# Performance work log

Hardware: AMD Instinct MI355X
Metric: run time of the kernel (lower is better)

The kernel has to match this reference:

```python
import jax, jax.numpy as jnp
import numpy as np

N_NODES = 50000


def _gcn_conv(h, src, dst, W, b):
    # h: [N, d_in] -> [N, d_out]; symmetric-normalized aggregation with self-loops
    N = h.shape[0]
    h = h @ W  # transform first (d_out < d_in), like PyG GCNConv
    deg = jax.ops.segment_sum(jnp.ones_like(dst, dtype=h.dtype), dst, num_segments=N)
    dinv = jnp.where(deg > 0, jax.lax.rsqrt(jnp.maximum(deg, 1.0)), 0.0)
    norm = dinv[src] * dinv[dst]  # [E']
    msg = h[src] * norm[:, None]  # [E', d_out]
    out = jax.ops.segment_sum(msg, dst, num_segments=N)
    return out + b


def setup_inputs() -> dict:
    key = jax.random.key(0)
    k1, k2, k3, k4 = jax.random.split(key, 4)
    dim_in, dim_h, dim_out, E = 512, 96, 40, 800000
    x = jax.random.normal(k1, (N_NODES, dim_in), dtype=jnp.float32)
    edge_index = jax.random.randint(k2, (2, E), 0, N_NODES, dtype=jnp.int64)
    W1 = jax.random.normal(k3, (dim_in, dim_h), dtype=jnp.float32) / np.sqrt(dim_in)
    b1 = jnp.zeros((dim_h,), dtype=jnp.float32)
    W2 = jax.random.normal(k4, (dim_h, dim_out), dtype=jnp.float32) / np.sqrt(dim_h)
    b2 = jnp.zeros((dim_out,), dtype=jnp.float32)
    return {"x": x, "edge_index": edge_index, "W1": W1, "b1": b1, "W2": W2, "b2": b2}


def reference(x, edge_index, W1, b1, W2, b2):
    N = x.shape[0]
    loops = jnp.arange(N, dtype=edge_index.dtype)
    src = jnp.concatenate([edge_index[0], loops])
    dst = jnp.concatenate([edge_index[1], loops])
    h = jax.nn.relu(_gcn_conv(x, src, dst, W1, b1))
    # dropout p=0.5 is identity in eval mode (training=False)
    logits = _gcn_conv(h, src, dst, W2, b2)
    return (logits, jax.nn.log_softmax(logits, axis=1))
```

## Files before the change

kernel.cpp:

```cpp
#include <hip/hip_runtime.h>
#include <hip/hip_bf16.h>
#include <cstdint>
#include <cstddef>

#define DIN 512
#define DH  96
#define DOUT 40

typedef __attribute__((ext_vector_type(8))) short s8v;
typedef __attribute__((ext_vector_type(4))) float f4v;

__device__ __forceinline__ ushort f2bf(float f) {
    uint u = __float_as_uint(f);
    u += 0x7fffu + ((u >> 16) & 1u);
    return (ushort)(u >> 16);
}
__device__ __forceinline__ uint f2bf2(float lo, float hi) {
    __hip_bfloat162 h = __float22bfloat162_rn(make_float2(lo, hi));
    return *(uint*)&h;
}
__device__ __forceinline__ float bflo(uint u) { return __uint_as_float(u << 16); }
__device__ __forceinline__ float bfhi(uint u) { return __uint_as_float(u & 0xffff0000u); }

__global__ __launch_bounds__(256) void k_prep(
    const float* __restrict__ W1, const float* __restrict__ W2,
    int* __restrict__ cnt, ushort* __restrict__ W1T, ushort* __restrict__ W2T, int N)
{
    int i = blockIdx.x * 256 + threadIdx.x;
    if (i < N) cnt[i] = 0;
    if (i < DIN * DH) {
        int k = i / DH, n = i % DH;
        W1T[(size_t)n * DIN + k] = f2bf(W1[i]);
    }
    if (i < 48 * DH) {
        int n = i / DH, k = i % DH;
        W2T[i] = (n < DOUT) ? f2bf(W2[(size_t)k * DOUT + n]) : (ushort)0;
    }
}

__global__ __launch_bounds__(256) void k_hist(
    const int* __restrict__ dst, int* __restrict__ cnt, int* __restrict__ pos, int E)
{
    int e = blockIdx.x * 256 + threadIdx.x;
    if (e < E) pos[e] = atomicAdd(&cnt[dst[e]], 1);
}

__global__ __launch_bounds__(256) void k_rowptr_all(
    const int* __restrict__ cnt, int* __restrict__ row_ptr,
    float* __restrict__ dinv, int N)
{
    __shared__ int p[256];
    __shared__ int wred[4];
    const int tid = threadIdx.x, b = blockIdx.x;

    int pre = 0;
    const int limit = b * 256;
    for (int j = tid; j < limit; j += 256) pre += cnt[j];
    #pragma unroll
    for (int off = 32; off >= 1; off >>= 1) pre += __shfl_down(pre, off, 64);
    if ((tid & 63) == 0) wred[tid >> 6] = pre;
    __syncthreads();
    const int base0 = wred[0] + wred[1] + wred[2] + wred[3];

    int i = b * 256 + tid;
    int c = (i < N) ? cnt[i] : 0;
    p[tid] = c;
    __syncthreads();
    #pragma unroll
    for (int off = 1; off < 256; off <<= 1) {
        int t = (tid >= off) ? p[tid - off] : 0;
        __syncthreads();
        p[tid] += t;
        __syncthreads();
    }
    int excl = p[tid] - c;
    if (i < N) {
        int base = base0 + excl;
        row_ptr[i] = base;
        dinv[i] = rsqrtf(1.0f + (float)c);
        if (i == N - 1) row_ptr[N] = base + c;
    }
}

__global__ __launch_bounds__(256) void k_fill(
    const int* __restrict__ src, const int* __restrict__ dst,
    const int* __restrict__ row_ptr, const int* __restrict__ pos,
    int* __restrict__ adj, int E)
{
    int e = blockIdx.x * 256 + threadIdx.x;
    if (e >= E) return;
    adj[row_ptr[dst[e]] + pos[e]] = src[e];
}

#define SWZ(r) (((r >> 1) & 3) << 3)
__global__ __launch_bounds__(256) void k_gemm1(
    const float* __restrict__ x, const ushort* __restrict__ W1T,
    const float* __restrict__ dinv, ushort* __restrict__ hs1, int N)
{
    __shared__ __align__(16) ushort lds[10240];
    const int tid = threadIdx.x;
    const int row0 = blockIdx.x * 64;
    const int lane = tid & 63, w = tid >> 6;
    const int rb = (w >> 1) * 32, cb = (w & 1) * 48;
    const int lm = lane & 15, lq = lane >> 4;

    int aof[2], bof[3];
    #pragma unroll
    for (int i = 0; i < 2; ++i) {
        int r = rb + i * 16 + lm;
        aof[i] = r * 32 + ((lq * 8) ^ SWZ(r));
    }
    #pragma unroll
    for (int j = 0; j < 3; ++j) {
        int n = cb + j * 16 + lm;
        bof[j] = 4096 + n * 32 + ((lq * 8) ^ SWZ(n));
    }

    f4v acc[2][3];
    #pragma unroll
    for (int i = 0; i < 2; ++i)
        #pragma unroll
        for (int j = 0; j < 3; ++j) acc[i][j] = (f4v)0.f;

    const int sr = tid >> 2;
    const int c0 = (tid & 3) * 8;

    auto stage = [&](int kt, int buf) {
        int k0 = kt * 32;
        int gr = row0 + sr;
        ushort* A = lds + buf * 2048;
        float4 v0 = make_float4(0.f, 0.f, 0.f, 0.f), v1 = v0;
        if (gr < N) {
            const float* pp = &x[(size_t)gr * DIN + k0 + c0];
            v0 = *(const float4*)pp;
            v1 = *(const float4*)(pp + 4);
        }
        uint4 wv;
        wv.x = f2bf2(v0.x, v0.y);
        wv.y = f2bf2(v0.z, v0.w);
        wv.z = f2bf2(v1.x, v1.y);
        wv.w = f2bf2(v1.z, v1.w);
        *(uint4*)&A[sr * 32 + (c0 ^ SWZ(sr))] = wv;
        ushort* B = lds + 4096 + buf * 3072;
        #pragma unroll
        for (int f = tid; f < 384; f += 256) {
            int n = f >> 2, cc = (f & 3) * 8;
            uint4 bv = *(const uint4*)&W1T[(size_t)n * DIN + k0 + cc];
            *(uint4*)&B[n * 32 + (cc ^ SWZ(n))] = bv;
        }
    };

    stage(0, 0);
    for (int kt = 0; kt < 16; ++kt) {
        __syncthreads();
        if (kt < 15) stage(kt + 1, (kt + 1) & 1);
        const int ab = (kt & 1) * 2048;
        const int bb = (kt & 1) * 3072;
        s8v b0 = *(s8v*)&lds[bof[0] + bb];
        s8v b1 = *(s8v*)&lds[bof[1] + bb];
        s8v b2 = *(s8v*)&lds[bof[2] + bb];
        #pragma unroll
        for (int i = 0; i < 2; ++i) {
            s8v a = *(s8v*)&lds[aof[i] + ab];
            acc[i][0] = __builtin_amdgcn_mfma_f32_16x16x32_bf16(a, b0, acc[i][0], 0, 0, 0);
            acc[i][1] = __builtin_amdgcn_mfma_f32_16x16x32_bf16(a, b1, acc[i][1], 0, 0, 0);
            acc[i][2] = __builtin_amdgcn_mfma_f32_16x16x32_bf16(a, b2, acc[i][2], 0, 0, 0);
        }
    }

    #pragma unroll
    for (int i = 0; i < 2; ++i) {
        int gr0 = row0 + rb + i * 16 + lq * 4;
        #pragma unroll
        for (int q = 0; q < 4; ++q) {
            int gr = gr0 + q;
            if (gr < N) {
                float di = dinv[gr];
                #pragma unroll
                for (int j = 0; j < 3; ++j)
                    hs1[(size_t)gr * DH + cb + j * 16 + lm] = f2bf(acc[i][j][q] * di);
            }
        }
    }
}

__global__ __launch_bounds__(256) void k_agg1(
    const int* __restrict__ row_ptr, const int* __restrict__ adj,
    const float* __restrict__ dinv, const ushort* __restrict__ hs1,
    const float* __restrict__ b1, ushort* __restrict__ h1, int N)
{
    int t = blockIdx.x * 256 + threadIdx.x;
    int node = t >> 6, lane = t & 63;
    if (node >= N) return;
    int c = lane << 1;
    const bool act = (c < DH);

    float a0 = 0.f, a1 = 0.f;
    if (act) {
        uint u = *(const uint*)&hs1[(size_t)node * DH + c];
        a0 = bflo(u); a1 = bfhi(u);
    }
    int e = row_ptr[node], e1 = row_ptr[node + 1];
    for (; e + 7 < e1; e += 8) {
        int s0 = adj[e],     s1 = adj[e + 1], s2 = adj[e + 2], s3 = adj[e + 3];
        int s4 = adj[e + 4], s5 = adj[e + 5], s6 = adj[e + 6], s7 = adj[e + 7];
        if (act) {
            uint u0 = *(const uint*)&hs1[(size_t)s0 * DH + c];
            uint u1 = *(const uint*)&hs1[(size_t)s1 * DH + c];
            uint u2 = *(const uint*)&hs1[(size_t)s2 * DH + c];
            uint u3 = *(const uint*)&hs1[(size_t)s3 * DH + c];
            uint u4 = *(const uint*)&hs1[(size_t)s4 * DH + c];
            uint u5 = *(const uint*)&hs1[(size_t)s5 * DH + c];
            uint u6 = *(const uint*)&hs1[(size_t)s6 * DH + c];
            uint u7 = *(const uint*)&hs1[(size_t)s7 * DH + c];
            a0 += bflo(u0); a1 += bfhi(u0);
            a0 += bflo(u1); a1 += bfhi(u1);
            a0 += bflo(u2); a1 += bfhi(u2);
            a0 += bflo(u3); a1 += bfhi(u3);
            a0 += bflo(u4); a1 += bfhi(u4);
            a0 += bflo(u5); a1 += bfhi(u5);
            a0 += bflo(u6); a1 += bfhi(u6);
            a0 += bflo(u7); a1 += bfhi(u7);
        }
    }
    for (; e < e1; ++e) {
        int s = adj[e];
        if (act) {
            uint u = *(const uint*)&hs1[(size_t)s * DH + c];
            a0 += bflo(u); a1 += bfhi(u);
        }
    }
    if (act) {
        float di = dinv[node];
        float r0 = fmaxf(fmaf(a0, di, b1[c]), 0.f);
        float r1 = fmaxf(fmaf(a1, di, b1[c + 1]), 0.f);
        *(uint*)&h1[(size_t)node * DH + c] = f2bf2(r0, r1);
    }
}

__global__ __launch_bounds__(256) void k_gemm2(
    const ushort* __restrict__ h1, const ushort* __restrict__ W2T,
    const float* __restrict__ dinv, ushort* __restrict__ hs2b, int N)
{
    __shared__ __align__(16) ushort lds[16384 + 48 * 128];
    const int tid = threadIdx.x;
    const int row0 = blockIdx.x * 128;

    for (int f = tid; f < 576; f += 256) {
        int r = f / 12, c = (f % 12) * 8;
        uint4 v = *(const uint4*)&W2T[r * DH + c];
        *(uint4*)&lds[16384 + r * 128 + (c ^ ((r & 7) << 3))] = v;
    }
    {
        int r = tid >> 1, half = tid & 1;
        int gr = row0 + r;
        #pragma unroll
        for (int i = 0; i < 6; ++i) {
            int c = half * 48 + i * 8;
            uint4 v = make_uint4(0, 0, 0, 0);
            if (gr < N) v = *(const uint4*)&h1[(size_t)gr * DH + c];
            *(uint4*)&lds[r * 128 + (c ^ ((r & 7) << 3))] = v;
        }
    }
    __syncthreads();

    const int lane = tid & 63, w = tid >> 6;
    const int rb = w * 32, lm = lane & 15, lq = lane >> 4;
    f4v acc[2][3];
    #pragma unroll
    for (int i = 0; i < 2; ++i)
        #pragma unroll
        for (int j = 0; j < 3; ++j) acc[i][j] = (f4v)0.f;

    #pragma unroll
    for (int ks = 0; ks < 3; ++ks) {
        int kk = ks * 32 + lq * 8;
        s8v b[3];
        #pragma unroll
        for (int j = 0; j < 3; ++j) {
            int n = j * 16 + lm;
            b[j] = *(s8v*)&lds[16384 + n * 128 + (kk ^ ((n & 7) << 3))];
        }
        #pragma unroll
        for (int i = 0; i < 2; ++i) {
            int r = rb + i * 16 + lm;
            s8v a = *(s8v*)&lds[r * 128 + (kk ^ ((r & 7) << 3))];
            #pragma unroll
            for (int j = 0; j < 3; ++j)
                acc[i][j] = __builtin_amdgcn_mfma_f32_16x16x32_bf16(a, b[j], acc[i][j], 0, 0, 0);
        }
    }

    #pragma unroll
    for (int i = 0; i < 2; ++i) {
        int gr0 = row0 + rb + i * 16 + lq * 4;
        #pragma unroll
        for (int q = 0; q < 4; ++q) {
            int gr = gr0 + q;
            if (gr < N) {
                float di = dinv[gr];
                #pragma unroll
                for (int j = 0; j < 3; ++j) {
                    int col = j * 16 + lm;
                    if (col < DOUT)
                        hs2b[(size_t)gr * 64 + col] = f2bf(acc[i][j][q] * di);
                }
            }
        }
    }
}

__global__ __launch_bounds__(256) void k_agg2sm(
    const int* __restrict__ row_ptr, const int* __restrict__ adj,
    const float* __restrict__ dinv, const ushort* __restrict__ hs2b,
    const float* __restrict__ b2, float* __restrict__ out,
    float* __restrict__ lsm, int N)
{
    int t = blockIdx.x * 256 + threadIdx.x;
    int node = t >> 6, lane = t & 63;
    if (node >= N) return;
    int c = lane << 1;
    const bool act = (c < DOUT);

    float a0 = 0.f, a1 = 0.f;
    if (act) {
        uint u = *(const uint*)&hs2b[(size_t)node * 64 + c];
        a0 = bflo(u); a1 = bfhi(u);
    }
    int e = row_ptr[node], e1 = row_ptr[node + 1];
    for (; e + 7 < e1; e += 8) {
        int s0 = adj[e],     s1 = adj[e + 1], s2 = adj[e + 2], s3 = adj[e + 3];
        int s4 = adj[e + 4], s5 = adj[e + 5], s6 = adj[e + 6], s7 = adj[e + 7];
        if (act) {
            uint u0 = *(const uint*)&hs2b[(size_t)s0 * 64 + c];
            uint u1 = *(const uint*)&hs2b[(size_t)s1 * 64 + c];
            uint u2 = *(const uint*)&hs2b[(size_t)s2 * 64 + c];
            uint u3 = *(const uint*)&hs2b[(size_t)s3 * 64 + c];
            uint u4 = *(const uint*)&hs2b[(size_t)s4 * 64 + c];
            uint u5 = *(const uint*)&hs2b[(size_t)s5 * 64 + c];
            uint u6 = *(const uint*)&hs2b[(size_t)s6 * 64 + c];
            uint u7 = *(const uint*)&hs2b[(size_t)s7 * 64 + c];
            a0 += bflo(u0); a1 += bfhi(u0);
            a0 += bflo(u1); a1 += bfhi(u1);
            a0 += bflo(u2); a1 += bfhi(u2);
            a0 += bflo(u3); a1 += bfhi(u3);
            a0 += bflo(u4); a1 += bfhi(u4);
            a0 += bflo(u5); a1 += bfhi(u5);
            a0 += bflo(u6); a1 += bfhi(u6);
            a0 += bflo(u7); a1 += bfhi(u7);
        }
    }
    for (; e < e1; ++e) {
        int s = adj[e];
        if (act) {
            uint u = *(const uint*)&hs2b[(size_t)s * 64 + c];
            a0 += bflo(u); a1 += bfhi(u);
        }
    }

    float di = act ? dinv[node] : 0.f;
    float v0 = act ? fmaf(a0, di, b2[c]) : -1e30f;
    float v1 = act ? fmaf(a1, di, b2[c + 1]) : -1e30f;
    float m = fmaxf(v0, v1);
    #pragma unroll
    for (int off = 32; off >= 1; off >>= 1) m = fmaxf(m, __shfl_xor(m, off));
    float ex = act ? (__expf(v0 - m) + __expf(v1 - m)) : 0.f;
    float s = ex;
    #pragma unroll
    for (int off = 32; off >= 1; off >>= 1) s += __shfl_xor(s, off);
    float lse = m + __logf(s);
    if (act) {
        *(float2*)&out[(size_t)node * DOUT + c] = make_float2(v0, v1);
        *(float2*)&lsm[(size_t)node * DOUT + c] = make_float2(v0 - lse, v1 - lse);
    }
}

extern "C" void kernel_launch(void* const* d_in, const int* in_sizes, int n_in,
                              void* d_out, int out_size, void* d_ws, size_t ws_size,
                              hipStream_t stream) {
    const float* x  = (const float*)d_in[0];
    const int*   ei = (const int*)d_in[1];
    const float* W1 = (const float*)d_in[2];
    const float* b1 = (const float*)d_in[3];
    const float* W2 = (const float*)d_in[4];
    const float* b2 = (const float*)d_in[5];

    const int N = in_sizes[0] / DIN;
    const int E = in_sizes[1] / 2;
    const int* srcp = ei;
    const int* dstp = ei + E;
    const int SB = (N + 255) / 256;

    ushort* hs1  = (ushort*)d_ws;
    ushort* h1   = hs1 + (size_t)N * DH;
    ushort* hs2b = h1 + (size_t)N * DH;
    float* dinv  = (float*)(hs2b + (size_t)N * 64);
    ushort* W1T  = (ushort*)(dinv + N);
    ushort* W2T  = W1T + (size_t)DH * DIN;
    int* cnt     = (int*)(W2T + 48 * DH);
    int* row_ptr = cnt + N;
    int* adj     = row_ptr + N + 1;
    int* pos     = adj + E;

    float* out = (float*)d_out;
    float* lsm = out + (size_t)N * DOUT;

    const int gE = (E + 255) / 256;

    k_prep<<<SB, 256, 0, stream>>>(W1, W2, cnt, W1T, W2T, N);
    k_hist<<<gE, 256, 0, stream>>>(dstp, cnt, pos, E);
    k_rowptr_all<<<SB, 256, 0, stream>>>(cnt, row_ptr, dinv, N);
    k_fill<<<gE, 256, 0, stream>>>(srcp, dstp, row_ptr, pos, adj, E);

    k_gemm1<<<(N + 63) / 64, 256, 0, stream>>>(x, W1T, dinv, hs1, N);
    k_agg1<<<(int)(((size_t)N * 64 + 255) / 256), 256, 0, stream>>>(row_ptr, adj, dinv, hs1, b1, h1, N);

    k_gemm2<<<(N + 127) / 128, 256, 0, stream>>>(h1, W2T, dinv, hs2b, N);
    k_agg2sm<<<(int)(((size_t)N * 64 + 255) / 256), 256, 0, stream>>>(row_ptr, adj, dinv, hs2b, b2, out, lsm, N);
}
```

Before: 203.8 us.

## Enlarge GEMM1 row tile to 128 and prefetch global tiles into registers

The first GEMM now covers 128 rows per block instead of 64, so each wave computes four 16-row MFMA tiles and every W1 tile staged in LDS is reused across twice as many rows. Global loads for the next k-step are issued into registers right after the barrier, and the bf16 conversion and LDS store happen at the start of the next iteration, so load latency overlaps the MFMA work. The cost is more registers per thread and fewer blocks (about 391 for 50k rows), which may leave part of the GPU underused.

```diff
diff --git a/kernel.cpp b/kernel.cpp
--- a/kernel.cpp
+++ b/kernel.cpp
@@ -97,70 +97,87 @@
     const float* __restrict__ x, const ushort* __restrict__ W1T,
     const float* __restrict__ dinv, ushort* __restrict__ hs1, int N)
 {
-    __shared__ __align__(16) ushort lds[10240];
+    __shared__ __align__(16) ushort lds[14336];
     const int tid = threadIdx.x;
-    const int row0 = blockIdx.x * 64;
+    const int row0 = blockIdx.x * 128;
     const int lane = tid & 63, w = tid >> 6;
-    const int rb = (w >> 1) * 32, cb = (w & 1) * 48;
+    const int rb = (w >> 1) * 64, cb = (w & 1) * 48;
     const int lm = lane & 15, lq = lane >> 4;
 
-    int aof[2], bof[3];
-    #pragma unroll
-    for (int i = 0; i < 2; ++i) {
+    int aof[4], bof[3];
+    #pragma unroll
+    for (int i = 0; i < 4; ++i) {
         int r = rb + i * 16 + lm;
         aof[i] = r * 32 + ((lq * 8) ^ SWZ(r));
     }
     #pragma unroll
     for (int j = 0; j < 3; ++j) {
         int n = cb + j * 16 + lm;
-        bof[j] = 4096 + n * 32 + ((lq * 8) ^ SWZ(n));
-    }
-
-    f4v acc[2][3];
-    #pragma unroll
-    for (int i = 0; i < 2; ++i)
+        bof[j] = 8192 + n * 32 + ((lq * 8) ^ SWZ(n));
+    }
+
+    f4v acc[4][3];
+    #pragma unroll
+    for (int i = 0; i < 4; ++i)
         #pragma unroll
         for (int j = 0; j < 3; ++j) acc[i][j] = (f4v)0.f;
 
-    const int sr = tid >> 2;
-    const int c0 = (tid & 3) * 8;
-
-    auto stage = [&](int kt, int buf) {
+    const int sr = tid >> 1, c0 = (tid & 1) * 16;
+    const int bn0 = tid >> 2, bc0 = (tid & 3) * 8;
+    const int bn1 = (tid + 256) >> 2, bc1 = (tid & 3) * 8;
+    const bool hasB1 = tid < 128;
+    const int gr = row0 + sr;
+    const bool grok = gr < N;
+
+    float4 ra[2][2];
+    uint4 rb0, rb1;
+
+    auto load_regs = [&](int kt) {
         int k0 = kt * 32;
-        int gr = row0 + sr;
-        ushort* A = lds + buf * 2048;
-        float4 v0 = make_float4(0.f, 0.f, 0.f, 0.f), v1 = v0;
-        if (gr < N) {
-            const float* pp = &x[(size_t)gr * DIN + k0 + c0];
-            v0 = *(const float4*)pp;
-            v1 = *(const float4*)(pp + 4);
-        }
-        uint4 wv;
-        wv.x = f2bf2(v0.x, v0.y);
-        wv.y = f2bf2(v0.z, v0.w);
-        wv.z = f2bf2(v1.x, v1.y);
-        wv.w = f2bf2(v1.z, v1.w);
-        *(uint4*)&A[sr * 32 + (c0 ^ SWZ(sr))] = wv;
-        ushort* B = lds + 4096 + buf * 3072;
-        #pragma unroll
-        for (int f = tid; f < 384; f += 256) {
-            int n = f >> 2, cc = (f & 3) * 8;
-            uint4 bv = *(const uint4*)&W1T[(size_t)n * DIN + k0 + cc];
-            *(uint4*)&B[n * 32 + (cc ^ SWZ(n))] = bv;
-        }
+        #pragma unroll
+        for (int s = 0; s < 2; ++s) {
+            if (grok) {
+                const float* pp = &x[(size_t)gr * DIN + k0 + c0 + s * 8];
+                ra[s][0] = *(const float4*)pp;
+                ra[s][1] = *(const float4*)(pp + 4);
+            } else {
+                ra[s][0] = make_float4(0.f, 0.f, 0.f, 0.f);
+                ra[s][1] = make_float4(0.f, 0.f, 0.f, 0.f);
+            }
+        }
+        rb0 = *(const uint4*)&W1T[(size_t)bn0 * DIN + k0 + bc0];
+        if (hasB1) rb1 = *(const uint4*)&W1T[(size_t)bn1 * DIN + k0 + bc1];
     };
-
-    stage(0, 0);
+    auto store_lds = [&](int buf) {
+        ushort* A = lds + buf * 4096;
+        #pragma unroll
+        for (int s = 0; s < 2; ++s) {
+            int c = c0 + s * 8;
+            uint4 wv;
+            wv.x = f2bf2(ra[s][0].x, ra[s][0].y);
+            wv.y = f2bf2(ra[s][0].z, ra[s][0].w);
+            wv.z = f2bf2(ra[s][1].x, ra[s][1].y);
+            wv.w = f2bf2(ra[s][1].z, ra[s][1].w);
+            *(uint4*)&A[sr * 32 + (c ^ SWZ(sr))] = wv;
+        }
+        ushort* B = lds + 8192 + buf * 3072;
+        *(uint4*)&B[bn0 * 32 + (bc0 ^ SWZ(bn0))] = rb0;
+        if (hasB1) *(uint4*)&B[bn1 * 32 + (bc1 ^ SWZ(bn1))] = rb1;
+    };
+
+    load_regs(0);
     for (int kt = 0; kt < 16; ++kt) {
+        const int buf = kt & 1;
+        store_lds(buf);
         __syncthreads();
-        if (kt < 15) stage(kt + 1, (kt + 1) & 1);
-        const int ab = (kt & 1) * 2048;
-        const int bb = (kt & 1) * 3072;
+        if (kt < 15) load_regs(kt + 1);
+        const int ab = buf * 4096;
+        const int bb = buf * 3072;
         s8v b0 = *(s8v*)&lds[bof[0] + bb];
         s8v b1 = *(s8v*)&lds[bof[1] + bb];
         s8v b2 = *(s8v*)&lds[bof[2] + bb];
         #pragma unroll
-        for (int i = 0; i < 2; ++i) {
+        for (int i = 0; i < 4; ++i) {
             s8v a = *(s8v*)&lds[aof[i] + ab];
             acc[i][0] = __builtin_amdgcn_mfma_f32_16x16x32_bf16(a, b0, acc[i][0], 0, 0, 0);
             acc[i][1] = __builtin_amdgcn_mfma_f32_16x16x32_bf16(a, b1, acc[i][1], 0, 0, 0);
@@ -169,16 +186,16 @@
     }
 
     #pragma unroll
-    for (int i = 0; i < 2; ++i) {
+    for (int i = 0; i < 4; ++i) {
         int gr0 = row0 + rb + i * 16 + lq * 4;
         #pragma unroll
         for (int q = 0; q < 4; ++q) {
-            int gr = gr0 + q;
-            if (gr < N) {
-                float di = dinv[gr];
+            int g = gr0 + q;
+            if (g < N) {
+                float di = dinv[g];
                 #pragma unroll
                 for (int j = 0; j < 3; ++j)
-                    hs1[(size_t)gr * DH + cb + j * 16 + lm] = f2bf(acc[i][j][q] * di);
+                    hs1[(size_t)g * DH + cb + j * 16 + lm] = f2bf(acc[i][j][q] * di);
             }
         }
     }
@@ -412,7 +429,7 @@
     k_rowptr_all<<<SB, 256, 0, stream>>>(cnt, row_ptr, dinv, N);
     k_fill<<<gE, 256, 0, stream>>>(srcp, dstp, row_ptr, pos, adj, E);
 
-    k_gemm1<<<(N + 63) / 64, 256, 0, stream>>>(x, W1T, dinv, hs1, N);
+    k_gemm1<<<(N + 127) / 128, 256, 0, stream>>>(x, W1T, dinv, hs1, N);
     k_agg1<<<(int)(((size_t)N * 64 + 255) / 256), 256, 0, stream>>>(row_ptr, adj, dinv, hs1, b1, h1, N);
 
     k_gemm2<<<(N + 127) / 128, 256, 0, stream>>>(h1, W2T, dinv, hs2b, N);
```

New measurement: 200.0 us. Within noise of the previous version (-1.9%).
